# Kernel optimization log

Measured on AMD Instinct MI355X. Metric: run time of the kernel, lower is better.

## Reference

```python
import jax, jax.numpy as jnp
import numpy as np
from jax import lax

B, T, K = 512, 1024, 48


def setup_inputs() -> dict:
    key = jax.random.key(0)
    k1, k2, k3, k4, k5, k6 = jax.random.split(key, 6)
    emissions = jax.random.normal(k1, (B, T, K), dtype=jnp.float32)
    lengths = jax.random.randint(k2, (B,), 1, T + 1)  # every seq has >=1 valid step
    raw_tags = jax.random.randint(k3, (B, T), 0, K)
    pos = jnp.arange(T)[None, :]
    tags = jnp.where(pos < lengths[:, None], raw_tags, -1)  # -1 = pad, as in pad_sequence
    u = lambda k, s: jax.random.uniform(k, s, minval=-0.1, maxval=0.1, dtype=jnp.float32)
    return {
        "emissions": emissions,
        "tags": tags,
        "start_transitions": u(k4, (K,)),
        "end_transitions": u(k5, (K,)),
        "transitions": u(k6, (K, K)),
    }


def _crf_loss(emissions, tags, mask, start_transitions, end_transitions, transitions):
    """-sum_b log p(tags_b | emissions_b)  (torchcrf reduction='sum')."""
    maskf = mask.astype(emissions.dtype)
    safe_tags = jnp.where(mask, tags, 0)
    b_idx = jnp.arange(emissions.shape[0])

    # ---- numerator: score of the gold path ----
    emit_scores = jnp.take_along_axis(emissions, safe_tags[:, :, None], axis=2)[..., 0]  # [B,T]
    trans_scores = transitions[safe_tags[:, :-1], safe_tags[:, 1:]]  # [B,T-1]
    score = start_transitions[safe_tags[:, 0]] + emit_scores[:, 0]
    score = score + jnp.sum((trans_scores + emit_scores[:, 1:]) * maskf[:, 1:], axis=1)
    lengths = mask.sum(axis=1)
    last_tags = safe_tags[b_idx, lengths - 1]
    score = score + end_transitions[last_tags]

    # ---- denominator: log partition via forward algorithm (scan over time) ----
    em_t = jnp.transpose(emissions, (1, 0, 2))  # [T,B,K]
    mk_t = jnp.transpose(mask, (1, 0))          # [T,B]

    def step(alpha, xm):
        e, m = xm  # e:[B,K], m:[B]
        nxt = jax.nn.logsumexp(alpha[:, :, None] + transitions[None], axis=1) + e
        return jnp.where(m[:, None], nxt, alpha), None

    alpha0 = start_transitions[None, :] + em_t[0]
    alpha, _ = lax.scan(step, alpha0, (em_t[1:], mk_t[1:]))
    log_z = jax.nn.logsumexp(alpha + end_transitions[None, :], axis=1)
    return -jnp.sum(score - log_z)


def _viterbi(emissions, mask, start_transitions, end_transitions, transitions):
    em_t = jnp.transpose(emissions, (1, 0, 2))  # [T,B,K]
    mk_t = jnp.transpose(mask, (1, 0))          # [T,B]
    ident = jnp.arange(K, dtype=jnp.int32)[None, :]  # identity backpointer for padded steps

    def vstep(alpha, xm):
        e, m = xm
        scores = alpha[:, :, None] + transitions[None]  # [B,K(prev),K(cur)]
        best_prev = jnp.argmax(scores, axis=1).astype(jnp.int32)  # [B,K]
        nxt = jnp.max(scores, axis=1) + e
        alpha2 = jnp.where(m[:, None], nxt, alpha)
        bp = jnp.where(m[:, None], best_prev, ident)
        return alpha2, bp

    alpha0 = start_transitions[None, :] + em_t[0]
    alpha, bps = lax.scan(vstep, alpha0, (em_t[1:], mk_t[1:]))  # bps: [T-1,B,K]
    best_last = jnp.argmax(alpha + end_transitions[None, :], axis=1).astype(jnp.int32)  # [B]

    def btstep(cur, bp):
        prev = jnp.take_along_axis(bp, cur[:, None], axis=1)[:, 0]
        return prev, cur

    first_tag, rest = lax.scan(btstep, best_last, bps, reverse=True)  # rest[t] = tag at t+1
    best_tags = jnp.concatenate([first_tag[None], rest], axis=0).T  # [B,T]
    return jnp.where(mask, best_tags, -1)


def reference(emissions, tags, start_transitions, end_transitions, transitions):
    mask = tags > -1
    loss = _crf_loss(emissions, tags, mask, start_transitions, end_transitions, transitions)
    pred_tags = _viterbi(emissions, mask, start_transitions, end_transitions, transitions)
    return loss, pred_tags
```

## Files before the change

kernel.cpp:

```cpp
#include <hip/hip_runtime.h>

#define BB 512
#define TT 1024
#define KK 48
#define RING 64
#define NINF (-1e30f)

#define CLOBBER() asm volatile("" ::: "memory")

__device__ __forceinline__ float rfirst(float v) {
    return __int_as_float(__builtin_amdgcn_readfirstlane(__float_as_int(v)));
}

#define MAXTREE(X, MV) {                                                     \
        float l1[16];                                                        \
        _Pragma("unroll")                                                    \
        for (int q_ = 0; q_ < 16; ++q_)                                      \
            l1[q_] = fmaxf(fmaxf(X[3 * q_], X[3 * q_ + 1]), X[3 * q_ + 2]);  \
        float l2[6];                                                         \
        _Pragma("unroll")                                                    \
        for (int q_ = 0; q_ < 5; ++q_)                                       \
            l2[q_] = fmaxf(fmaxf(l1[3 * q_], l1[3 * q_ + 1]),                \
                           l1[3 * q_ + 2]);                                  \
        l2[5] = l1[15];                                                      \
        MV = fmaxf(fmaxf(fmaxf(l2[0], l2[1]), l2[2]),                        \
                   fmaxf(fmaxf(l2[3], l2[4]), l2[5]));                       \
    }

#define XADDS(R4, X) {                                                       \
        _Pragma("unroll")                                                    \
        for (int q_ = 0; q_ < 12; ++q_) {                                    \
            float4 v_ = R4[q_];                                              \
            X[4 * q_ + 0] = v_.x + Tc[4 * q_ + 0];                           \
            X[4 * q_ + 1] = v_.y + Tc[4 * q_ + 1];                           \
            X[4 * q_ + 2] = v_.z + Tc[4 * q_ + 2];                           \
            X[4 * q_ + 3] = v_.w + Tc[4 * q_ + 3];                           \
        }                                                                    \
    }

#define ARGKEY(X, MV, BI) {                                                  \
        unsigned u[KK];                                                      \
        _Pragma("unroll")                                                    \
        for (int i_ = 0; i_ < KK; ++i_)                                      \
            u[i_] = (unsigned)__float_as_int(X[i_] - MV) | (unsigned)i_;     \
        unsigned m1[16];                                                     \
        _Pragma("unroll")                                                    \
        for (int q_ = 0; q_ < 16; ++q_)                                      \
            m1[q_] = min(min(u[3 * q_], u[3 * q_ + 1]), u[3 * q_ + 2]);      \
        unsigned m2[6];                                                      \
        _Pragma("unroll")                                                    \
        for (int q_ = 0; q_ < 5; ++q_)                                       \
            m2[q_] = min(min(m1[3 * q_], m1[3 * q_ + 1]), m1[3 * q_ + 2]);   \
        m2[5] = m1[15];                                                      \
        BI = min(min(min(m2[0], m2[1]), m2[2]),                              \
                 min(min(m2[3], m2[4]), m2[5]));                             \
    }

__global__ __launch_bounds__(256, 2) void crf_pc(
    const float* __restrict__ em, const int* __restrict__ tags,
    const float* __restrict__ st, const float* __restrict__ en,
    const float* __restrict__ tr, float* __restrict__ out,
    float* __restrict__ wsl)
{
    __shared__ unsigned char s_bp[TT * KK];
    __shared__ unsigned char s_path[TT];
    __shared__ __align__(16) float s_ring[RING][64];
    __shared__ __align__(16) float s_favb[64];
    __shared__ int s_flag, s_c0, s_c1;

    const int b    = blockIdx.x;
    const int tid  = threadIdx.x;
    const int lane = tid & 63;
    const int wid  = tid >> 6;

    const float* emb = em + (size_t)b * TT * KK;
    const int*   tgb = tags + (size_t)b * TT;

    if (tid == 0) { s_flag = -1; s_c0 = 0; s_c1 = 0; }

    int cnt = 0;
    for (int t = lane; t < TT; t += 64) cnt += (tgb[t] > -1) ? 1 : 0;
#pragma unroll
    for (int off = 32; off >= 1; off >>= 1) cnt += __shfl_xor(cnt, off);
    const int len = cnt;

    const bool act = lane < KK;
    const int  jj  = act ? lane : (KK - 1);
    const int  S   = len - 1;

    __syncthreads();

    float av_final = NINF;

    if (wid == 0) {
        float sc = 0.f;
        for (int t = lane; t < len; t += 64) {
            int tg = tgb[t];
            sc += emb[t * KK + tg];
            if (t > 0) sc += tr[tgb[t - 1] * KK + tg];
        }
#pragma unroll
        for (int off = 32; off >= 1; off >>= 1) sc += __shfl_xor(sc, off);
        const float score = sc + st[tgb[0]] + en[tgb[len - 1]];

        float eTc[KK];
#pragma unroll
        for (int i = 0; i < KK; ++i) eTc[i] = __expf(tr[i * KK + jj]);

        float a0 = st[jj] + emb[jj];
        float C  = rfirst(a0);
        float p  = __expf(a0 - C);

        const float4* S4 = (const float4*)(&s_favb[0]);

        float e[2];
        {
            int t1 = (1 < len) ? 1 : (len - 1);
            int t2 = (2 < len) ? 2 : (len - 1);
            e[1] = emb[(size_t)t1 * KK + jj];
            e[0] = emb[(size_t)t2 * KK + jj];
        }

#define FSTEP(t_, RENORM) {                                                  \
        const float eS = e[(t_) & 1];                                        \
        s_favb[lane] = p;                       \
        float z0 = 0.f, z1 = 0.f, z2 = 0.f, z3 = 0.f;                        \
        float z4 = 0.f, z5 = 0.f, z6 = 0.f, z7 = 0.f;                        \
        _Pragma("unroll")                                                    \
        for (int q_ = 0; q_ < 6; ++q_) {                                     \
            float4 v0 = S4[2 * q_], v1 = S4[2 * q_ + 1];                     \
            z0 = fmaf(v0.x, eTc[8 * q_ + 0], z0);                            \
            z1 = fmaf(v0.y, eTc[8 * q_ + 1], z1);                            \
            z2 = fmaf(v0.z, eTc[8 * q_ + 2], z2);                            \
            z3 = fmaf(v0.w, eTc[8 * q_ + 3], z3);                            \
            z4 = fmaf(v1.x, eTc[8 * q_ + 4], z4);                            \
            z5 = fmaf(v1.y, eTc[8 * q_ + 5], z5);                            \
            z6 = fmaf(v1.z, eTc[8 * q_ + 6], z6);                            \
            z7 = fmaf(v1.w, eTc[8 * q_ + 7], z7);                            \
        }                                                                    \
        p = (((z0 + z1) + (z2 + z3)) + ((z4 + z5) + (z6 + z7)))              \
            * __expf(eS);                                                    \
        if (RENORM) {                                                        \
            float m_ = rfirst(p);                                            \
            p *= __frcp_rn(m_);                                              \
            C += __logf(m_);                                                 \
        }                                                                    \
        int tn = (t_) + 2; tn = (tn < len) ? tn : (len - 1);                 \
        e[(t_) & 1] = emb[(size_t)tn * KK + jj];                             \
    }
        {
            int t = 1;
            for (; t + 4 <= S + 1; t += 4) {
                FSTEP(t, 0) FSTEP(t + 1, 0) FSTEP(t + 2, 0) FSTEP(t + 3, 1)
            }
            for (; t <= S; ++t) FSTEP(t, 1)
        }
#undef FSTEP

        float y = act ? (p * __expf(en[jj])) : 0.f;
#pragma unroll
        for (int off = 32; off >= 1; off >>= 1) y += __shfl_xor(y, off);
        float logz = C + __logf(y);
        if (lane == 0) wsl[b] = score - logz;
    } else if (wid == 1) {
        __builtin_amdgcn_s_setprio(1);
        float Tc[KK];
#pragma unroll
        for (int i = 0; i < KK; ++i) Tc[i] = tr[i * KK + jj];

        float av = st[jj] + emb[jj];

        *(volatile float*)&s_ring[0][lane] = av;
        CLOBBER();
        if (lane == 0) *(volatile int*)&s_flag = 0;
        CLOBBER();

        float e[2];
        {
            int t1 = (1 < len) ? 1 : (len - 1);
            int t2 = (2 < len) ? 2 : (len - 1);
            e[1] = emb[(size_t)t1 * KK + jj];
            e[0] = emb[(size_t)t2 * KK + jj];
        }

#define PSTEP(t_, PAR) {                                                     \
        const float4* R4 =                                                   \
            (const float4*)(&s_ring[((t_) - 1) & (RING - 1)][0]);            \
        float X[KK];                                                         \
        XADDS(R4, X)                                                         \
        float M; MAXTREE(X, M)                                               \
        av = M + e[PAR];                                                     \
        CLOBBER();                                                           \
        *(volatile float*)&s_ring[(t_) & (RING - 1)][lane] = av;             \
        CLOBBER();                                                           \
        int tn = (t_) + 2; tn = (tn < len) ? tn : (len - 1);                 \
        e[PAR] = emb[(size_t)tn * KK + jj];                                  \
    }

        int t = 1;
        for (; t + 1 <= S; t += 2) {
            if ((t & 31) == 1) {
                while (min(*(volatile int*)&s_c0,
                           *(volatile int*)&s_c1) < t - 31) { CLOBBER(); }
                CLOBBER();
            }
            PSTEP(t, 1) PSTEP(t + 1, 0)
            if (lane == 0) *(volatile int*)&s_flag = t + 1;
            CLOBBER();
        }
        if (t <= S) {
            PSTEP(t, 1)
            if (lane == 0) *(volatile int*)&s_flag = t;
            CLOBBER();
        }
#undef PSTEP
        __builtin_amdgcn_s_setprio(0);
        av_final = av;
    } else {
        float Tc[KK];
#pragma unroll
        for (int i = 0; i < KK; ++i) Tc[i] = tr[i * KK + jj];

        const int start = (wid == 2) ? 1 : 2;
        volatile int* cslot = (wid == 2) ? (volatile int*)&s_c0
                                         : (volatile int*)&s_c1;

        for (int tau = start; tau <= S; tau += 2) {
            const int want = tau - 1;
            while (*(volatile int*)&s_flag < want) { CLOBBER(); }
            CLOBBER();
            const float4* R4 =
                (const float4*)(&s_ring[(tau - 1) & (RING - 1)][0]);
            float X[KK];
            XADDS(R4, X)
            float M; MAXTREE(X, M)
            unsigned bi; ARGKEY(X, M, bi)
            s_bp[tau * KK + jj] = (unsigned char)bi;
            CLOBBER();
            if (lane == 0) *cslot = tau;
            CLOBBER();
        }
    }

    __syncthreads();

    if (wid == 1) {
        float v = act ? (av_final + en[jj]) : NINF;
        float M = v;
#pragma unroll
        for (int off = 32; off >= 1; off >>= 1) M = fmaxf(M, __shfl_xor(M, off));
        unsigned long long msk = __ballot(v == M);
        int cur = __ffsll(msk) - 1;
        s_path[len - 1] = (unsigned char)cur;

        int t = len - 1;
        while (t >= 1) {
            const int n = (t < 8) ? t : 8;
            unsigned r[8];
#pragma unroll
            for (int k = 0; k < 8; ++k)
                r[k] = (k < n) ? (unsigned)s_bp[(t - k) * KK + jj] : 0u;
#pragma unroll
            for (int k = 0; k < 8; ++k) {
                if (k < n) {
                    cur = __builtin_amdgcn_readlane((int)r[k], cur);
                    if (lane == 0) s_path[t - k - 1] = (unsigned char)cur;
                }
            }
            t -= n;
        }

        float* ob = out + 1 + (size_t)b * TT;
        for (int tt = lane; tt < TT; tt += 64)
            ob[tt] = (tt < len) ? (float)s_path[tt] : -1.0f;
    }
}

__global__ __launch_bounds__(512) void loss_reduce(const float* __restrict__ ws,
                                                   float* __restrict__ out)
{
    __shared__ float sh[8];
    const int lane = threadIdx.x & 63;
    const int w    = threadIdx.x >> 6;
    float s = ws[threadIdx.x];
#pragma unroll
    for (int off = 32; off >= 1; off >>= 1) s += __shfl_xor(s, off);
    if (lane == 0) sh[w] = s;
    __syncthreads();
    if (threadIdx.x == 0) {
        float tot = 0.f;
        for (int i = 0; i < 8; ++i) tot += sh[i];
        out[0] = -tot;
    }
}

extern "C" void kernel_launch(void* const* d_in, const int* in_sizes, int n_in,
                              void* d_out, int out_size, void* d_ws, size_t ws_size,
                              hipStream_t stream)
{
    const float* em   = (const float*)d_in[0];
    const int*   tags = (const int*)d_in[1];
    const float* st   = (const float*)d_in[2];
    const float* en   = (const float*)d_in[3];
    const float* tr   = (const float*)d_in[4];
    float* out = (float*)d_out;
    float* wsl = (float*)d_ws;

    hipLaunchKernelGGL(crf_pc, dim3(BB), dim3(256), 0, stream,
                       em, tags, st, en, tr, out, wsl);
    hipLaunchKernelGGL(loss_reduce, dim3(1), dim3(512), 0, stream, wsl, out);
}
```

Measured before the change: 475.6 us.

## Widen to six argmax consumer waves and publish per-step max for reuse

Blocks grow from 4 to 8 waves: one forward wave, one Viterbi max-producer wave and six consumer waves that each handle every sixth timestep for backpointer argmax. The producer now writes the per-step max into a second ring, so consumers skip their own max tree and only compute the argmax key. Consumers spin with s_sleep, and the producer publishes a flag every step rather than every two and throttles every 16 steps against all six consumer counters. The ring shrinks to 32 entries. The aim is to take the backpointer work off the producer's critical path, at the cost of more waves per block, finer-grained synchronisation traffic and possible register and occupancy pressure from launch_bounds(512,4).

New measurement: 671.9 us. 41.3% more time.

```diff
diff --git a/kernel.cpp b/kernel.cpp
--- a/kernel.cpp
+++ b/kernel.cpp
@@ -3,7 +3,7 @@
 #define BB 512
 #define TT 1024
 #define KK 48
-#define RING 64
+#define RING 32
 #define NINF (-1e30f)
 
 #define CLOBBER() asm volatile("" ::: "memory")
@@ -56,7 +56,7 @@
                  min(min(m2[3], m2[4]), m2[5]));                             \
     }
 
-__global__ __launch_bounds__(256, 2) void crf_pc(
+__global__ __launch_bounds__(512, 4) void crf_pc(
     const float* __restrict__ em, const int* __restrict__ tags,
     const float* __restrict__ st, const float* __restrict__ en,
     const float* __restrict__ tr, float* __restrict__ out,
@@ -65,8 +65,10 @@
     __shared__ unsigned char s_bp[TT * KK];
     __shared__ unsigned char s_path[TT];
     __shared__ __align__(16) float s_ring[RING][64];
+    __shared__ __align__(16) float s_mring[RING][64];
     __shared__ __align__(16) float s_favb[64];
-    __shared__ int s_flag, s_c0, s_c1;
+    __shared__ int s_flag;
+    __shared__ int s_cc[6];
 
     const int b    = blockIdx.x;
     const int tid  = threadIdx.x;
@@ -76,7 +78,8 @@
     const float* emb = em + (size_t)b * TT * KK;
     const int*   tgb = tags + (size_t)b * TT;
 
-    if (tid == 0) { s_flag = -1; s_c0 = 0; s_c1 = 0; }
+    if (tid == 0) s_flag = 0;
+    if (tid < 6)  s_cc[tid] = 0;
 
     int cnt = 0;
     for (int t = lane; t < TT; t += 64) cnt += (tgb[t] > -1) ? 1 : 0;
@@ -172,8 +175,6 @@
 
         *(volatile float*)&s_ring[0][lane] = av;
         CLOBBER();
-        if (lane == 0) *(volatile int*)&s_flag = 0;
-        CLOBBER();
 
         float e[2];
         {
@@ -183,37 +184,32 @@
             e[0] = emb[(size_t)t2 * KK + jj];
         }
 
-#define PSTEP(t_, PAR) {                                                     \
-        const float4* R4 =                                                   \
-            (const float4*)(&s_ring[((t_) - 1) & (RING - 1)][0]);            \
-        float X[KK];                                                         \
-        XADDS(R4, X)                                                         \
-        float M; MAXTREE(X, M)                                               \
-        av = M + e[PAR];                                                     \
-        CLOBBER();                                                           \
-        *(volatile float*)&s_ring[(t_) & (RING - 1)][lane] = av;             \
-        CLOBBER();                                                           \
-        int tn = (t_) + 2; tn = (tn < len) ? tn : (len - 1);                 \
-        e[PAR] = emb[(size_t)tn * KK + jj];                                  \
-    }
-
-        int t = 1;
-        for (; t + 1 <= S; t += 2) {
-            if ((t & 31) == 1) {
-                while (min(*(volatile int*)&s_c0,
-                           *(volatile int*)&s_c1) < t - 31) { CLOBBER(); }
+        volatile int* cc = (volatile int*)s_cc;
+        for (int t = 1; t <= S; ++t) {
+            if ((t & 15) == 1 && t > 16) {
+                for (;;) {
+                    int m0 = min(min(cc[0], cc[1]), min(cc[2], cc[3]));
+                    int m1 = min(cc[4], cc[5]);
+                    if (min(m0, m1) >= t - 16) break;
+                    CLOBBER();
+                }
                 CLOBBER();
             }
-            PSTEP(t, 1) PSTEP(t + 1, 0)
-            if (lane == 0) *(volatile int*)&s_flag = t + 1;
-            CLOBBER();
-        }
-        if (t <= S) {
-            PSTEP(t, 1)
+            const float4* R4 =
+                (const float4*)(&s_ring[(t - 1) & (RING - 1)][0]);
+            float X[KK];
+            XADDS(R4, X)
+            float M; MAXTREE(X, M)
+            av = M + e[t & 1];
+            CLOBBER();
+            *(volatile float*)&s_ring[t & (RING - 1)][lane]  = av;
+            *(volatile float*)&s_mring[t & (RING - 1)][lane] = M;
+            CLOBBER();
             if (lane == 0) *(volatile int*)&s_flag = t;
             CLOBBER();
-        }
-#undef PSTEP
+            int tn = t + 2; tn = (tn < len) ? tn : (len - 1);
+            e[t & 1] = emb[(size_t)tn * KK + jj];
+        }
         __builtin_amdgcn_s_setprio(0);
         av_final = av;
     } else {
@@ -221,25 +217,26 @@
 #pragma unroll
         for (int i = 0; i < KK; ++i) Tc[i] = tr[i * KK + jj];
 
-        const int start = (wid == 2) ? 1 : 2;
-        volatile int* cslot = (wid == 2) ? (volatile int*)&s_c0
-                                         : (volatile int*)&s_c1;
-
-        for (int tau = start; tau <= S; tau += 2) {
-            const int want = tau - 1;
-            while (*(volatile int*)&s_flag < want) { CLOBBER(); }
+        const int start = wid - 1;
+        volatile int* cslot = (volatile int*)&s_cc[wid - 2];
+
+        for (int tau = start; tau <= S; tau += 6) {
+            while (*(volatile int*)&s_flag < tau)
+                __builtin_amdgcn_s_sleep(1);
             CLOBBER();
             const float4* R4 =
                 (const float4*)(&s_ring[(tau - 1) & (RING - 1)][0]);
             float X[KK];
             XADDS(R4, X)
-            float M; MAXTREE(X, M)
+            float M = *(volatile float*)&s_mring[tau & (RING - 1)][lane];
             unsigned bi; ARGKEY(X, M, bi)
             s_bp[tau * KK + jj] = (unsigned char)bi;
             CLOBBER();
             if (lane == 0) *cslot = tau;
             CLOBBER();
         }
+        if (lane == 0) *cslot = TT + 1;
+        CLOBBER();
     }
 
     __syncthreads();
@@ -306,7 +303,7 @@
     float* out = (float*)d_out;
     float* wsl = (float*)d_ws;
 
-    hipLaunchKernelGGL(crf_pc, dim3(BB), dim3(256), 0, stream,
+    hipLaunchKernelGGL(crf_pc, dim3(BB), dim3(512), 0, stream,
                        em, tags, st, en, tr, out, wsl);
     hipLaunchKernelGGL(loss_reduce, dim3(1), dim3(512), 0, stream, wsl, out);
 }
```
